# Performance work log

Measured on AMD Instinct MI355X. Metric: run time of the kernel, lower is better.

## Reference

```python
import jax, jax.numpy as jnp
import numpy as np

HID = 256
STYLE_DIM = 64
NUM_STYLES = 8
IN_DIM = 3 + STYLE_DIM


def setup_inputs() -> dict:
    key = jax.random.key(0)
    ks = jax.random.split(key, 12)
    B, H, W = 2, 512, 512
    rgb = jax.random.uniform(ks[0], (B, 3, H, W), dtype=jnp.float32)
    style_idx = jax.random.randint(ks[1], (B,), 0, NUM_STYLES, dtype=jnp.int32)
    # style embedding table (torch init: normal std=0.01)
    emb_table = 0.01 * jax.random.normal(ks[2], (NUM_STYLES, STYLE_DIM), dtype=jnp.float32)
    # kaiming-normal (fan_in, relu gain sqrt(2)) weights stored as [in, out]
    def kaiming(k, fan_in, fan_out):
        std = np.sqrt(2.0 / fan_in)
        return std * jax.random.normal(k, (fan_in, fan_out), dtype=jnp.float32)
    W0 = kaiming(ks[3], IN_DIM, HID); b0 = jnp.zeros((HID,), jnp.float32)
    W1 = kaiming(ks[4], HID, HID);    b1 = jnp.zeros((HID,), jnp.float32)
    W2 = kaiming(ks[5], HID, HID);    b2 = jnp.zeros((HID,), jnp.float32)
    W3 = kaiming(ks[6], HID, 3);      b3 = jnp.zeros((3,), jnp.float32)
    return {"rgb": rgb, "style_idx": style_idx, "emb_table": emb_table,
            "W0": W0, "b0": b0, "W1": W1, "b1": b1,
            "W2": W2, "b2": b2, "W3": W3, "b3": b3}


def reference(rgb, style_idx, emb_table, W0, b0, W1, b1, W2, b2, W3, b3):
    B, C, H, W_ = rgb.shape  # CHW image input
    # [B,3,H,W] -> [B*H*W, 3]
    rgb_flat = jnp.transpose(rgb, (0, 2, 3, 1)).reshape(-1, 3)
    # style embedding lookup, broadcast per pixel
    emb = emb_table[style_idx]                              # [B, style_dim]
    emb = jnp.broadcast_to(emb[:, None, :], (B, H * W_, STYLE_DIM)).reshape(-1, STYLE_DIM)
    x = jnp.concatenate([rgb_flat, emb], axis=-1)           # [N, 67]
    gelu = lambda t: jax.nn.gelu(t, approximate=False)      # torch nn.GELU default (erf)
    x = gelu(x @ W0 + b0)
    x = gelu(x @ W1 + b1)
    x = gelu(x @ W2 + b2)
    out_flat = jax.nn.sigmoid(x @ W3 + b3)                  # [N, 3]
    out = out_flat.reshape(B, H, W_, 3).transpose(0, 3, 1, 2)
    return out
```

## Files before the change

### kernel.cpp

```cpp
#include <hip/hip_runtime.h>

#define HW  (512*512)

typedef _Float16 half8  __attribute__((__vector_size__(16)));
typedef _Float16 half4  __attribute__((__vector_size__(8)));
typedef _Float16 half2_t __attribute__((__vector_size__(4)));
typedef float    floatx4 __attribute__((__vector_size__(16)));

__device__ __forceinline__ float gelu_f(float x){
    float x2 = x * x;
    float q  = __builtin_fmaf(x2, -0.1029432f, -2.3022079f);
    float e  = __builtin_amdgcn_exp2f(x * q);
    return x * __builtin_amdgcn_rcpf(1.0f + e);
}

__device__ __forceinline__ float sigmoid_f(float x){
    float e = __builtin_amdgcn_exp2f(-1.44269504f * x);
    return __builtin_amdgcn_rcpf(1.0f + e);
}


__global__ void prep_all(const float* __restrict__ W1, const float* __restrict__ W2,
                         const float* __restrict__ W3, const float* __restrict__ emb,
                         const int* __restrict__ sidx, const float* __restrict__ W0,
                         const float* __restrict__ b0,
                         _Float16* __restrict__ wp, float* __restrict__ c0){
    __shared__ float ld[32][68];
    int blk = blockIdx.x;
    int tid = threadIdx.x;
    if (blk < 64){
        int mat = blk >> 5;
        int g   = blk & 31;
        int ks  = g >> 2;
        int ntq = g & 3;
        const float* W = mat ? W2 : W1;
        int row = tid >> 3;
        int c8  = (tid & 7) * 8;
        const float* src = &W[(ks*32 + row)*256 + ntq*64 + c8];
        *(floatx4*)&ld[row][c8]     = *(const floatx4*)src;
        *(floatx4*)&ld[row][c8 + 4] = *(const floatx4*)(src + 4);
        __syncthreads();
        int lane = tid & 63;
        int nt_l = tid >> 6;
        half8 h;
        #pragma unroll
        for (int j = 0; j < 8; j++)
            h[j] = (_Float16)ld[(lane >> 4)*8 + j][nt_l*16 + (lane & 15)];
        _Float16* dst = wp + mat*65536 + (ks*16 + ntq*4 + nt_l)*512 + lane*8;
        *(half8*)dst = h;
    } else if (blk < 80){
        int i    = (blk - 64)*256 + tid;
        int j    = i & 7;
        int lane = (i >> 3) & 63;
        int ks   = i >> 9;
        int k = ks*32 + ((lane >> 4) << 3) + j;
        int n = lane & 15;
        wp[131072 + i] = (_Float16)((n < 3) ? W3[k*3 + n] : 0.0f);
    } else {
        int b = blk - 80;
        int s = sidx[b];
        float acc = b0[tid];
        #pragma unroll 8
        for (int d = 0; d < 64; d++)
            acc = fmaf(emb[s*64 + d], W0[(3 + d)*256 + tid], acc);
        c0[b*256 + tid] = acc;
    }
}

__device__ __forceinline__ floatx4 mfma16(half8 a, half8 b, floatx4 c){
    return __builtin_amdgcn_mfma_f32_16x16x32_f16(a, b, c, 0, 0, 0);
}

__global__ __launch_bounds__(256, 5)
void nilut_main(const float* __restrict__ rgb,
                const float* __restrict__ W0,
                const float* __restrict__ b1v,
                const float* __restrict__ b2v,
                const float* __restrict__ b3v,
                const _Float16* __restrict__ wp,
                const float* __restrict__ c0,
                float* __restrict__ out){
    __shared__ __align__(16) _Float16 act[64 * 256];
    float* actf = (float*)act;

    const int tid = threadIdx.x;
    const int wg  = blockIdx.x;
    const int pixbase = wg * 64;
    const int b   = pixbase >> 18;
    const int hw0 = pixbase & (HW - 1);

    #pragma unroll
    for (int r = 0; r < 4; r++){
        int q = r*256 + tid;
        actf[q] = (q < 768) ? W0[q] : c0[b*256 + (q - 768)];
    }
    __syncthreads();

    const int ng = tid & 31, rg = tid >> 5;
    floatx4 cw[4][2];
    #pragma unroll
    for (int p = 0; p < 4; p++){
        cw[p][0] = *(const floatx4*)&actf[p*256 + ng*8];
        cw[p][1] = *(const floatx4*)&actf[p*256 + ng*8 + 4];
    }
    __syncthreads();

    #pragma unroll
    for (int hf = 0; hf < 2; hf++){
        floatx4 rv[3];
        #pragma unroll
        for (int c = 0; c < 3; c++)
            rv[c] = *(const floatx4*)&rgb[b*3*HW + c*HW + hw0 + rg*8 + hf*4];
        #pragma unroll
        for (int r4 = 0; r4 < 4; r4++){
            int px = rg*8 + hf*4 + r4;
            float rr = rv[0][r4], gg = rv[1][r4], bb = rv[2][r4];
            half8 v;
            #pragma unroll
            for (int j = 0; j < 8; j++){
                int hi = j >> 2, lo = j & 3;
                float z = fmaf(rr, cw[0][hi][lo],
                          fmaf(gg, cw[1][hi][lo],
                          fmaf(bb, cw[2][hi][lo], cw[3][hi][lo])));
                v[j] = (_Float16)gelu_f(z);
            }
            *(half8*)&act[px*256 + ((ng ^ (px & 7)) << 3)] = v;
        }
    }
    __syncthreads();

    const int lane = tid & 63;
    const int wv   = tid >> 6;
    const int ln15 = lane & 15;
    const int quad = lane >> 4;
    const int qr   = quad * 4;
    const int sx   = ln15 & 7;
    const int qx8  = (quad ^ (sx & 3)) * 8;
    const int kb32 = ((sx >> 2) & 1) << 5;
    const int qh   = quad >> 1, qs = (quad & 1) * 4;

    int pbq[4], eb[4];
    #pragma unroll
    for (int pt = 0; pt < 4; pt++){
        pbq[pt] = (pt*16 + ln15)*256 + qx8;
        eb[pt]  = (pt*16 + ln15)*256 + qs;
    }

    const _Float16* wl  = wp;
    const float* bias   = b1v;
    #pragma unroll 1
    for (int L = 0; L < 2; L++){
        floatx4 acc[4][4];
        #pragma unroll
        for (int mtl = 0; mtl < 4; mtl++){
            floatx4 bv = *(const floatx4*)&bias[(wv*4 + mtl)*16 + qr];
            #pragma unroll
            for (int pt = 0; pt < 4; pt++)
                acc[pt][mtl] = bv;
        }

        const half8* wp8 = (const half8*)wl;
        #pragma unroll 2
        for (int ks = 0; ks < 8; ks++){
            int t = (ks << 5) ^ kb32;
            half8 bfr[4];
            #pragma unroll
            for (int pt = 0; pt < 4; pt++)
                bfr[pt] = *(const half8*)&act[pbq[pt] + t];
            #pragma unroll
            for (int mtl = 0; mtl < 4; mtl++){
                half8 af = wp8[(ks*16 + wv*4 + mtl)*64 + lane];
                #pragma unroll
                for (int pt = 0; pt < 4; pt++)
                    acc[pt][mtl] = mfma16(af, bfr[pt], acc[pt][mtl]);
            }
        }
        __syncthreads();
        #pragma unroll
        for (int mtl = 0; mtl < 4; mtl++){
            int cx = (((wv*4 + mtl)*2 + qh) ^ sx) << 3;
            #pragma unroll
            for (int pt = 0; pt < 4; pt++){
                floatx4 v = acc[pt][mtl];
                half2_t g01 = __builtin_amdgcn_cvt_pkrtz(gelu_f(v[0]), gelu_f(v[1]));
                half2_t g23 = __builtin_amdgcn_cvt_pkrtz(gelu_f(v[2]), gelu_f(v[3]));
                half4 h;
                h[0] = g01[0]; h[1] = g01[1]; h[2] = g23[0]; h[3] = g23[1];
                *(half4*)&act[eb[pt] + cx] = h;
            }
        }
        __syncthreads();
        wl = wp + 65536;
        bias = b2v;
    }

    {
        const half8* wp8 = (const half8*)(wp + 131072);
        floatx4 ac = (floatx4){0.f,0.f,0.f,0.f};
        int pb = (wv*16 + ln15)*256 + qx8;
        #pragma unroll
        for (int ks = 0; ks < 8; ks++){
            half8 bfr = *(const half8*)&act[pb + ((ks << 5) ^ kb32)];
            half8 af  = wp8[ks*64 + lane];
            ac = mfma16(af, bfr, ac);
        }
        __syncthreads();
        if (quad == 0){
            #pragma unroll
            for (int r = 0; r < 3; r++)
                actf[r*64 + wv*16 + ln15] = sigmoid_f(ac[r] + b3v[r]);
        }
        __syncthreads();
        if (tid < 48){
            int c  = tid >> 4;
            int i2 = tid & 15;
            float4* dst = (float4*)(out + (b*3 + c)*HW + hw0);
            dst[i2] = ((float4*)(actf + c*64))[i2];
        }
    }
}

extern "C" void kernel_launch(void* const* d_in, const int* in_sizes, int n_in,
                              void* d_out, int out_size, void* d_ws, size_t ws_size,
                              hipStream_t stream){
    const float* rgb = (const float*)d_in[0];
    const int*  sidx = (const int*) d_in[1];
    const float* emb = (const float*)d_in[2];
    const float* W0  = (const float*)d_in[3];
    const float* b0  = (const float*)d_in[4];
    const float* W1  = (const float*)d_in[5];
    const float* b1  = (const float*)d_in[6];
    const float* W2  = (const float*)d_in[7];
    const float* b2  = (const float*)d_in[8];
    const float* W3  = (const float*)d_in[9];
    const float* b3  = (const float*)d_in[10];
    float* out = (float*)d_out;

    _Float16* wp = (_Float16*)d_ws;
    float*    c0 = (float*)((char*)d_ws + 270336);

    int n_pix = in_sizes[0] / 3;
    prep_all<<<82, 256, 0, stream>>>(W1, W2, W3, emb, sidx, W0, b0, wp, c0);
    nilut_main<<<n_pix / 64, 256, 0, stream>>>(rgb, W0, b1, b2, b3, wp, c0, out);
}
```

Before: 281.8 us.

## Halve pixels per workgroup and double-buffer activations to drop a barrier

Each workgroup now processes 32 pixels instead of 64, with the LDS activation buffer split into two 32-pixel halves that alternate between read and write across layers. This removes the barrier between the MFMA loop and the GELU writeback and gives more, smaller workgroups for occupancy. In exchange, each weight fragment loaded from global memory is reused across only two pixel tiles instead of four, which doubles weight traffic per pixel. Half the waves also sit idle in the final layer.

```diff
diff --git a/kernel.cpp b/kernel.cpp
--- a/kernel.cpp
+++ b/kernel.cpp
@@ -80,12 +80,13 @@
                 const _Float16* __restrict__ wp,
                 const float* __restrict__ c0,
                 float* __restrict__ out){
-    __shared__ __align__(16) _Float16 act[64 * 256];
+    __shared__ __align__(16) _Float16 act[2 * 32 * 256];
     float* actf = (float*)act;
+    const int BUF = 32 * 256;
 
     const int tid = threadIdx.x;
     const int wg  = blockIdx.x;
-    const int pixbase = wg * 64;
+    const int pixbase = wg * 32;
     const int b   = pixbase >> 18;
     const int hw0 = pixbase & (HW - 1);
 
@@ -105,15 +106,14 @@
     }
     __syncthreads();
 
-    #pragma unroll
-    for (int hf = 0; hf < 2; hf++){
+    {
         floatx4 rv[3];
         #pragma unroll
         for (int c = 0; c < 3; c++)
-            rv[c] = *(const floatx4*)&rgb[b*3*HW + c*HW + hw0 + rg*8 + hf*4];
+            rv[c] = *(const floatx4*)&rgb[b*3*HW + c*HW + hw0 + rg*4];
         #pragma unroll
         for (int r4 = 0; r4 < 4; r4++){
-            int px = rg*8 + hf*4 + r4;
+            int px = rg*4 + r4;
             float rr = rv[0][r4], gg = rv[1][r4], bb = rv[2][r4];
             half8 v;
             #pragma unroll
@@ -139,57 +139,53 @@
     const int kb32 = ((sx >> 2) & 1) << 5;
     const int qh   = quad >> 1, qs = (quad & 1) * 4;
 
-    int pbq[4], eb[4];
+    int pbq[2], eb[2];
     #pragma unroll
-    for (int pt = 0; pt < 4; pt++){
+    for (int pt = 0; pt < 2; pt++){
         pbq[pt] = (pt*16 + ln15)*256 + qx8;
         eb[pt]  = (pt*16 + ln15)*256 + qs;
     }
 
     const _Float16* wl  = wp;
     const float* bias   = b1v;
+    int rbuf = 0, wbuf = BUF;
     #pragma unroll 1
     for (int L = 0; L < 2; L++){
-        floatx4 acc[4][4];
+        floatx4 acc[2][4];
         #pragma unroll
         for (int mtl = 0; mtl < 4; mtl++){
             floatx4 bv = *(const floatx4*)&bias[(wv*4 + mtl)*16 + qr];
-            #pragma unroll
-            for (int pt = 0; pt < 4; pt++)
-                acc[pt][mtl] = bv;
+            acc[0][mtl] = bv; acc[1][mtl] = bv;
         }
 
         const half8* wp8 = (const half8*)wl;
         #pragma unroll 2
         for (int ks = 0; ks < 8; ks++){
             int t = (ks << 5) ^ kb32;
-            half8 bfr[4];
-            #pragma unroll
-            for (int pt = 0; pt < 4; pt++)
-                bfr[pt] = *(const half8*)&act[pbq[pt] + t];
+            half8 bf0 = *(const half8*)&act[rbuf + pbq[0] + t];
+            half8 bf1 = *(const half8*)&act[rbuf + pbq[1] + t];
             #pragma unroll
             for (int mtl = 0; mtl < 4; mtl++){
                 half8 af = wp8[(ks*16 + wv*4 + mtl)*64 + lane];
-                #pragma unroll
-                for (int pt = 0; pt < 4; pt++)
-                    acc[pt][mtl] = mfma16(af, bfr[pt], acc[pt][mtl]);
-            }
-        }
-        __syncthreads();
+                acc[0][mtl] = mfma16(af, bf0, acc[0][mtl]);
+                acc[1][mtl] = mfma16(af, bf1, acc[1][mtl]);
+            }
+        }
         #pragma unroll
         for (int mtl = 0; mtl < 4; mtl++){
             int cx = (((wv*4 + mtl)*2 + qh) ^ sx) << 3;
             #pragma unroll
-            for (int pt = 0; pt < 4; pt++){
+            for (int pt = 0; pt < 2; pt++){
                 floatx4 v = acc[pt][mtl];
                 half2_t g01 = __builtin_amdgcn_cvt_pkrtz(gelu_f(v[0]), gelu_f(v[1]));
                 half2_t g23 = __builtin_amdgcn_cvt_pkrtz(gelu_f(v[2]), gelu_f(v[3]));
                 half4 h;
                 h[0] = g01[0]; h[1] = g01[1]; h[2] = g23[0]; h[3] = g23[1];
-                *(half4*)&act[eb[pt] + cx] = h;
+                *(half4*)&act[wbuf + eb[pt] + cx] = h;
             }
         }
         __syncthreads();
+        int tmp = rbuf; rbuf = wbuf; wbuf = tmp;
         wl = wp + 65536;
         bias = b2v;
     }
@@ -197,25 +193,27 @@
     {
         const half8* wp8 = (const half8*)(wp + 131072);
         floatx4 ac = (floatx4){0.f,0.f,0.f,0.f};
-        int pb = (wv*16 + ln15)*256 + qx8;
-        #pragma unroll
-        for (int ks = 0; ks < 8; ks++){
-            half8 bfr = *(const half8*)&act[pb + ((ks << 5) ^ kb32)];
-            half8 af  = wp8[ks*64 + lane];
-            ac = mfma16(af, bfr, ac);
+        if (wv < 2){
+            int pb = rbuf + (wv*16 + ln15)*256 + qx8;
+            #pragma unroll
+            for (int ks = 0; ks < 8; ks++){
+                half8 bfr = *(const half8*)&act[pb + ((ks << 5) ^ kb32)];
+                half8 af  = wp8[ks*64 + lane];
+                ac = mfma16(af, bfr, ac);
+            }
+        }
+        float* bounce = (float*)&act[wbuf];
+        if (wv < 2 && quad == 0){
+            #pragma unroll
+            for (int r = 0; r < 3; r++)
+                bounce[r*32 + wv*16 + ln15] = sigmoid_f(ac[r] + b3v[r]);
         }
         __syncthreads();
-        if (quad == 0){
-            #pragma unroll
-            for (int r = 0; r < 3; r++)
-                actf[r*64 + wv*16 + ln15] = sigmoid_f(ac[r] + b3v[r]);
-        }
-        __syncthreads();
-        if (tid < 48){
-            int c  = tid >> 4;
-            int i2 = tid & 15;
+        if (tid < 24){
+            int c  = tid >> 3;
+            int i2 = tid & 7;
             float4* dst = (float4*)(out + (b*3 + c)*HW + hw0);
-            dst[i2] = ((float4*)(actf + c*64))[i2];
+            dst[i2] = ((float4*)(bounce + c*32))[i2];
         }
     }
 }
@@ -241,5 +239,5 @@
 
     int n_pix = in_sizes[0] / 3;
     prep_all<<<82, 256, 0, stream>>>(W1, W2, W3, emb, sidx, W0, b0, wp, c0);
-    nilut_main<<<n_pix / 64, 256, 0, stream>>>(rgb, W0, b1, b2, b3, wp, c0, out);
-}
+    nilut_main<<<n_pix / 32, 256, 0, stream>>>(rgb, W0, b1, b2, b3, wp, c0, out);
+}
```

Result: slower. 318.5 us (+13.0%).
